# Performance work log

Measured on AMD Instinct MI355X. Metric: run time of the kernel, lower is better.

Reference implementation:

```python
import jax, jax.numpy as jnp
import numpy as np

NUM_BLOCKS = 10  # dilation doubling cycle
NUM_LAYERS = 4   # total blocks = 40


def _dconv(x, w, b, d):
    """Causal dilated conv1d, kernel=2. x:[B,C,T], w:[O,I,2] -> [B,O,T].
    Torch pads (d,d) then slices off the last d frames == left-pad by d."""
    y = jax.lax.conv_general_dilated(
        x, w, window_strides=(1,), padding=[(d, 0)], rhs_dilation=(d,),
        dimension_numbers=("NCH", "OIH", "NCH"))
    return y + b[:, None]


def _pw(x, w, b):
    """1x1 conv. x:[B,I,T], w:[O,I,1] -> [B,O,T]."""
    return jnp.einsum("oi,bit->bot", w[:, :, 0], x) + b[:, None]


def setup_inputs() -> dict:
    key = jax.random.key(0)
    ks = jax.random.split(key, 16)
    s = 0.05
    return {
        "x": jax.random.normal(ks[0], (8, 256, 16384), jnp.float32),
        "in_w": jax.random.normal(ks[1], (32, 256, 1), jnp.float32) * s,
        "in_b": jax.random.normal(ks[2], (32,), jnp.float32) * s,
        "conv_w": jax.random.normal(ks[3], (40, 32, 32, 2), jnp.float32) * s,
        "conv_b": jax.random.normal(ks[4], (40, 32), jnp.float32) * s,
        "gate_w": jax.random.normal(ks[5], (40, 32, 32, 2), jnp.float32) * s,
        "gate_b": jax.random.normal(ks[6], (40, 32), jnp.float32) * s,
        "res_w": jax.random.normal(ks[7], (40, 32, 32, 1), jnp.float32) * s,
        "res_b": jax.random.normal(ks[8], (40, 32), jnp.float32) * s,
        "skip_w": jax.random.normal(ks[9], (40, 32, 32, 1), jnp.float32) * s,
        "skip_b": jax.random.normal(ks[10], (40, 32), jnp.float32) * s,
        "s1_w": jax.random.normal(ks[11], (32, 32, 1), jnp.float32) * s,
        "s1_b": jax.random.normal(ks[12], (32,), jnp.float32) * s,
        "s2_w": jax.random.normal(ks[13], (256, 32, 1), jnp.float32) * s,
        "s2_b": jax.random.normal(ks[14], (256,), jnp.float32) * s,
    }


def reference(x, in_w, in_b, conv_w, conv_b, gate_w, gate_b,
              res_w, res_b, skip_w, skip_b, s1_w, s1_b, s2_w, s2_b):
    h = _pw(x, in_w, in_b)  # [B,32,T]
    skip_sum = jnp.zeros_like(h)
    for i in range(NUM_LAYERS * NUM_BLOCKS):
        d = 2 ** (i % NUM_BLOCKS)
        a = jnp.tanh(_dconv(h, conv_w[i], conv_b[i], d)) * \
            jax.nn.sigmoid(_dconv(h, gate_w[i], gate_b[i], d))
        h = h + _pw(a, res_w[i], res_b[i])
        skip_sum = skip_sum + _pw(a, skip_w[i], skip_b[i])
    out = jax.nn.relu(_pw(skip_sum, s1_w, s1_b))
    out = _pw(out, s2_w, s2_b)  # [B,256,T]
    return out
```

## Files before the change

### kernel.cpp

```cpp
#include <hip/hip_runtime.h>

#define T_LEN 16384

typedef _Float16 f16;
typedef f16 f16x8 __attribute__((ext_vector_type(8)));
typedef float f32x4 __attribute__((ext_vector_type(4)));

__device__ __forceinline__ float fast_exp2(float x) { return __builtin_amdgcn_exp2f(x); }
__device__ __forceinline__ float fast_rcp(float x)  { return __builtin_amdgcn_rcpf(x); }
__device__ __forceinline__ float fast_tanh(float x) {
  return 1.f - 2.f * fast_rcp(1.f + fast_exp2(x * 2.885390081777927f));
}
__device__ __forceinline__ float fast_sig(float x) {
  return fast_rcp(1.f + fast_exp2(-x * 1.4426950408889634f));
}

__device__ __forceinline__ f32x4 mfma16(f16x8 a, f16x8 b, f32x4 c) {
  return __builtin_amdgcn_mfma_f32_16x16x32_f16(a, b, c, 0, 0, 0);
}

struct h2s { f16 hi, lo; };
__device__ __forceinline__ h2s split(float v) {
  h2s r; r.hi = (f16)v; r.lo = (f16)(v - (float)r.hi); return r;
}


__global__ __launch_bounds__(256, 2) void in_k(
    const float* __restrict__ x, const float* __restrict__ w,
    const float* __restrict__ bias, float4* __restrict__ h, float4* __restrict__ skip)
{
  __shared__ float4 W[256][8];
  __shared__ float B[32];
  const int tid = threadIdx.x;
  for (int i = tid; i < 2048; i += 256) {
    int c = i >> 3, o4 = i & 7;
    W[c][o4] = make_float4(w[(o4*4+0)*256 + c], w[(o4*4+1)*256 + c],
                           w[(o4*4+2)*256 + c], w[(o4*4+3)*256 + c]);
  }
  if (tid < 32) B[tid] = bias[tid];
  __syncthreads();

  const int idx = blockIdx.x * 256 + tid;
  const int b = idx >> 14;
  const int t = idx & (T_LEN - 1);
  const float* xb = x + (size_t)b * 256 * T_LEN + t;

  float acc[32];
  #pragma unroll
  for (int o = 0; o < 32; o++) acc[o] = B[o];
  #pragma unroll 4
  for (int c = 0; c < 256; c++) {
    float v = xb[(size_t)c * T_LEN];
    #pragma unroll
    for (int o4 = 0; o4 < 8; o4++) {
      float4 ww = W[c][o4];
      acc[o4*4+0] += ww.x * v; acc[o4*4+1] += ww.y * v;
      acc[o4*4+2] += ww.z * v; acc[o4*4+3] += ww.w * v;
    }
  }
  #pragma unroll
  for (int j = 0; j < 8; j++) {
    size_t p = ((size_t)(b * 8 + j) << 14) + t;
    h[p]    = make_float4(acc[j*4+0], acc[j*4+1], acc[j*4+2], acc[j*4+3]);
    skip[p] = make_float4(0.f, 0.f, 0.f, 0.f);
  }
}

__global__ __launch_bounds__(256, 1) void layer_k(
    const float4* __restrict__ hin, float4* __restrict__ hout, float4* __restrict__ skip,
    const float* __restrict__ cw, const float* __restrict__ cb,
    const float* __restrict__ gw, const float* __restrict__ gb,
    const float* __restrict__ rw, const float* __restrict__ rb,
    const float* __restrict__ sw, const float* __restrict__ sb, int d)
{
  const int tid  = threadIdx.x;
  const int lane = tid & 63;
  const int g    = lane >> 4;
  const int m16  = lane & 15;

  f16x8 wch[2][2], wcl[2][2], wgh[2][2], wgl[2][2];
  f16x8 wrh[2], wrl[2], wsh[2], wsl[2];
  f32x4 cbv[2], gbv[2], rbv[2], sbv[2];
  #pragma unroll
  for (int mt = 0; mt < 2; mt++) {
    const int o = mt*16 + m16;
    const float4* cp = (const float4*)&cw[(o*32 + 8*g)*2];
    const float4* gp = (const float4*)&gw[(o*32 + 8*g)*2];
    float4 c0=cp[0], c1=cp[1], c2=cp[2], c3=cp[3];
    float4 g0=gp[0], g1=gp[1], g2=gp[2], g3=gp[3];
    float4 r0 = *(const float4*)&rw[o*32 + 8*g];
    float4 r1 = *(const float4*)&rw[o*32 + 8*g + 4];
    float4 s0 = *(const float4*)&sw[o*32 + 8*g];
    float4 s1 = *(const float4*)&sw[o*32 + 8*g + 4];
    float cc[16] = {c0.x,c0.y,c0.z,c0.w, c1.x,c1.y,c1.z,c1.w,
                    c2.x,c2.y,c2.z,c2.w, c3.x,c3.y,c3.z,c3.w};
    float gg[16] = {g0.x,g0.y,g0.z,g0.w, g1.x,g1.y,g1.z,g1.w,
                    g2.x,g2.y,g2.z,g2.w, g3.x,g3.y,g3.z,g3.w};
    float rr[8] = {r0.x,r0.y,r0.z,r0.w, r1.x,r1.y,r1.z,r1.w};
    float ss[8] = {s0.x,s0.y,s0.z,s0.w, s1.x,s1.y,s1.z,s1.w};
    #pragma unroll
    for (int i = 0; i < 8; i++) {
      h2s t0 = split(cc[2*i+0]); wch[mt][0][i]=t0.hi; wcl[mt][0][i]=t0.lo;
      h2s t1 = split(cc[2*i+1]); wch[mt][1][i]=t1.hi; wcl[mt][1][i]=t1.lo;
      h2s u0 = split(gg[2*i+0]); wgh[mt][0][i]=u0.hi; wgl[mt][0][i]=u0.lo;
      h2s u1 = split(gg[2*i+1]); wgh[mt][1][i]=u1.hi; wgl[mt][1][i]=u1.lo;
      h2s vr = split(rr[i]);     wrh[mt][i]=vr.hi;    wrl[mt][i]=vr.lo;
      h2s vs = split(ss[i]);     wsh[mt][i]=vs.hi;    wsl[mt][i]=vs.lo;
    }
    cbv[mt] = *(const f32x4*)&cb[mt*16 + 4*g];
    gbv[mt] = *(const f32x4*)&gb[mt*16 + 4*g];
    rbv[mt] = *(const f32x4*)&rb[mt*16 + 4*g];
    sbv[mt] = *(const f32x4*)&sb[mt*16 + 4*g];
  }

  const int wid   = (blockIdx.x << 2) | (tid >> 6);
  const int tile0 = wid << 2;

  float4 Bst[2][4];
  {
    const int b = tile0 >> 10;
    const int tcol = ((tile0 << 4) & (T_LEN-1)) + m16;
    const size_t cbase = ((size_t)b << 17) + (size_t)tcol;
    Bst[0][0] = hin[cbase + ((size_t)(2*g)   << 14)];
    Bst[0][1] = hin[cbase + ((size_t)(2*g+1) << 14)];
    float4 z = make_float4(0.f,0.f,0.f,0.f);
    Bst[0][2] = z; Bst[0][3] = z;
    if (tcol >= d) {
      Bst[0][2] = hin[cbase - (size_t)d + ((size_t)(2*g)   << 14)];
      Bst[0][3] = hin[cbase - (size_t)d + ((size_t)(2*g+1) << 14)];
    }
  }

  #pragma unroll
  for (int k = 0; k < 4; k++) {
    const int tile = tile0 + k;
    const int b = tile >> 10;
    const int tcol = ((tile << 4) & (T_LEN-1)) + m16;
    const size_t cbase = ((size_t)b << 17) + (size_t)tcol;
    const int cur = k & 1, nxt = cur ^ 1;

    float4 hr0 = hin[cbase  + ((size_t)g     << 14)];
    float4 hr1 = hin[cbase  + ((size_t)(4+g) << 14)];
    float4 sv0 = skip[cbase + ((size_t)g     << 14)];
    float4 sv1 = skip[cbase + ((size_t)(4+g) << 14)];

    f16x8 bth, btl, bdh, bdl;
    {
      float tv[8] = {Bst[cur][0].x,Bst[cur][0].y,Bst[cur][0].z,Bst[cur][0].w,
                     Bst[cur][1].x,Bst[cur][1].y,Bst[cur][1].z,Bst[cur][1].w};
      float dv[8] = {Bst[cur][2].x,Bst[cur][2].y,Bst[cur][2].z,Bst[cur][2].w,
                     Bst[cur][3].x,Bst[cur][3].y,Bst[cur][3].z,Bst[cur][3].w};
      #pragma unroll
      for (int i = 0; i < 8; i++) {
        h2s a = split(tv[i]); bth[i]=a.hi; btl[i]=a.lo;
        h2s c = split(dv[i]); bdh[i]=c.hi; bdl[i]=c.lo;
      }
    }

    if (k < 3) {
      const int tn = tile + 1;
      const int bn = tn >> 10;
      const int tcn = ((tn << 4) & (T_LEN-1)) + m16;
      const size_t cbn = ((size_t)bn << 17) + (size_t)tcn;
      Bst[nxt][0] = hin[cbn + ((size_t)(2*g)   << 14)];
      Bst[nxt][1] = hin[cbn + ((size_t)(2*g+1) << 14)];
      float4 z = make_float4(0.f,0.f,0.f,0.f);
      Bst[nxt][2] = z; Bst[nxt][3] = z;
      if (tcn >= d) {
        Bst[nxt][2] = hin[cbn - (size_t)d + ((size_t)(2*g)   << 14)];
        Bst[nxt][3] = hin[cbn - (size_t)d + ((size_t)(2*g+1) << 14)];
      }
    }

    f32x4 pa[2], ga[2];
    #pragma unroll
    for (int mt = 0; mt < 2; mt++) {
      f32x4 p = {0.f,0.f,0.f,0.f};
      p = mfma16(wch[mt][0], bdh, p);
      p = mfma16(wcl[mt][0], bdh, p);
      p = mfma16(wch[mt][0], bdl, p);
      p = mfma16(wch[mt][1], bth, p);
      p = mfma16(wcl[mt][1], bth, p);
      p = mfma16(wch[mt][1], btl, p);
      pa[mt] = p;
      f32x4 q = {0.f,0.f,0.f,0.f};
      q = mfma16(wgh[mt][0], bdh, q);
      q = mfma16(wgl[mt][0], bdh, q);
      q = mfma16(wgh[mt][0], bdl, q);
      q = mfma16(wgh[mt][1], bth, q);
      q = mfma16(wgl[mt][1], bth, q);
      q = mfma16(wgh[mt][1], btl, q);
      ga[mt] = q;
    }

    float av0[4], av1[4];
    #pragma unroll
    for (int r = 0; r < 4; r++) {
      av0[r] = fast_tanh(pa[0][r] + cbv[0][r]) * fast_sig(ga[0][r] + gbv[0][r]);
      av1[r] = fast_tanh(pa[1][r] + cbv[1][r]) * fast_sig(ga[1][r] + gbv[1][r]);
    }

    f16x8 bah, bal;
    #pragma unroll
    for (int i = 0; i < 8; i++) {
      int srcl = (((2*g + (i>>2)) & 3) << 4) | m16;
      float v0 = __shfl(av0[i&3], srcl, 64);
      float v1 = __shfl(av1[i&3], srcl, 64);
      float v = (g >= 2) ? v1 : v0;
      h2s s = split(v); bah[i]=s.hi; bal[i]=s.lo;
    }

    f32x4 ra[2], sa[2];
    #pragma unroll
    for (int mt = 0; mt < 2; mt++) {
      f32x4 p = {0.f,0.f,0.f,0.f};
      p = mfma16(wrh[mt], bah, p);
      p = mfma16(wrl[mt], bah, p);
      p = mfma16(wrh[mt], bal, p);
      ra[mt] = p;
      f32x4 q = {0.f,0.f,0.f,0.f};
      q = mfma16(wsh[mt], bah, q);
      q = mfma16(wsl[mt], bah, q);
      q = mfma16(wsh[mt], bal, q);
      sa[mt] = q;
    }

    #pragma unroll
    for (int mt = 0; mt < 2; mt++) {
      size_t qidx = cbase + ((size_t)(4*mt + g) << 14);
      float4 hr = (mt == 0) ? hr0 : hr1;
      float4 sv = (mt == 0) ? sv0 : sv1;
      hout[qidx] = make_float4(hr.x + rbv[mt][0] + ra[mt][0],
                               hr.y + rbv[mt][1] + ra[mt][1],
                               hr.z + rbv[mt][2] + ra[mt][2],
                               hr.w + rbv[mt][3] + ra[mt][3]);
      skip[qidx] = make_float4(sv.x + sbv[mt][0] + sa[mt][0],
                               sv.y + sbv[mt][1] + sa[mt][1],
                               sv.z + sbv[mt][2] + sa[mt][2],
                               sv.w + sbv[mt][3] + sa[mt][3]);
    }
  }
}

__global__ __launch_bounds__(256, 2) void out_k(
    const float4* __restrict__ skip,
    const float* __restrict__ w1, const float* __restrict__ b1,
    const float* __restrict__ w2, const float* __restrict__ b2,
    float* __restrict__ out)
{
  __shared__ float4 W1[32][8];
  __shared__ float4 W2[32][64];
  __shared__ float B1[32];
  __shared__ float B2[256];
  const int tid = threadIdx.x;
  {
    int ic = tid >> 3, o4 = tid & 7;
    W1[ic][o4] = make_float4(w1[(o4*4+0)*32+ic], w1[(o4*4+1)*32+ic],
                             w1[(o4*4+2)*32+ic], w1[(o4*4+3)*32+ic]);
  }
  for (int e = tid; e < 2048; e += 256) {
    int ic = e >> 6, o4 = e & 63;
    W2[ic][o4] = make_float4(w2[(o4*4+0)*32+ic], w2[(o4*4+1)*32+ic],
                             w2[(o4*4+2)*32+ic], w2[(o4*4+3)*32+ic]);
  }
  B2[tid & 255] = b2[tid & 255];
  if (tid < 32) B1[tid] = b1[tid];
  __syncthreads();

  const int idx = blockIdx.x * 256 + tid;
  const int b = idx >> 14;
  const int t = idx & (T_LEN - 1);
  const size_t base = ((size_t)b * 8 << 14) + t;

  float sk[32];
  #pragma unroll
  for (int j = 0; j < 8; j++) {
    float4 v = skip[base + ((size_t)j << 14)];
    sk[j*4+0]=v.x; sk[j*4+1]=v.y; sk[j*4+2]=v.z; sk[j*4+3]=v.w;
  }

  float r[32];
  #pragma unroll
  for (int o = 0; o < 32; o++) r[o] = B1[o];
  #pragma unroll
  for (int ic = 0; ic < 32; ic++) {
    float v = sk[ic];
    #pragma unroll
    for (int o4 = 0; o4 < 8; o4++) {
      float4 w = W1[ic][o4];
      r[o4*4+0] += w.x * v; r[o4*4+1] += w.y * v;
      r[o4*4+2] += w.z * v; r[o4*4+3] += w.w * v;
    }
  }
  #pragma unroll
  for (int o = 0; o < 32; o++) r[o] = fmaxf(r[o], 0.f);

  float* ob = out + (size_t)b * 256 * T_LEN + t;
  #pragma unroll 2
  for (int o4 = 0; o4 < 64; o4++) {
    float a0 = B2[o4*4+0], a1 = B2[o4*4+1], a2 = B2[o4*4+2], a3 = B2[o4*4+3];
    #pragma unroll
    for (int ic = 0; ic < 32; ic++) {
      float4 w = W2[ic][o4];
      float v = r[ic];
      a0 += w.x * v; a1 += w.y * v; a2 += w.z * v; a3 += w.w * v;
    }
    ob[(size_t)(o4*4+0)*T_LEN] = a0;
    ob[(size_t)(o4*4+1)*T_LEN] = a1;
    ob[(size_t)(o4*4+2)*T_LEN] = a2;
    ob[(size_t)(o4*4+3)*T_LEN] = a3;
  }
}

extern "C" void kernel_launch(void* const* d_in, const int* in_sizes, int n_in,
                              void* d_out, int out_size, void* d_ws, size_t ws_size,
                              hipStream_t stream)
{
  const float* x    = (const float*)d_in[0];
  const float* in_w = (const float*)d_in[1];
  const float* in_b = (const float*)d_in[2];
  const float* cw   = (const float*)d_in[3];
  const float* cb   = (const float*)d_in[4];
  const float* gw   = (const float*)d_in[5];
  const float* gb   = (const float*)d_in[6];
  const float* rw   = (const float*)d_in[7];
  const float* rb   = (const float*)d_in[8];
  const float* sw   = (const float*)d_in[9];
  const float* sb   = (const float*)d_in[10];
  const float* w1   = (const float*)d_in[11];
  const float* b1   = (const float*)d_in[12];
  const float* w2   = (const float*)d_in[13];
  const float* b2   = (const float*)d_in[14];
  float* out = (float*)d_out;

  float4* h0   = (float4*)out;
  float4* h1   = (float4*)(out + 4194304);
  float4* skip = (float4*)d_ws;

  dim3 blk(256);
  in_k<<<dim3(512), blk, 0, stream>>>(x, in_w, in_b, h0, skip);

  float4* ha = h0;
  float4* hb = h1;
  for (int l = 0; l < 40; l++) {
    int d = 1 << (l % 10);
    layer_k<<<dim3(512), blk, 0, stream>>>(ha, hb, skip,
        cw + (size_t)l * 2048, cb + l * 32,
        gw + (size_t)l * 2048, gb + l * 32,
        rw + (size_t)l * 1024, rb + l * 32,
        sw + (size_t)l * 1024, sb + l * 32, d);
    float4* tmp = ha; ha = hb; hb = tmp;
  }

  out_k<<<dim3(512), blk, 0, stream>>>(skip, w1, b1, w2, b2, out);
}
```

Baseline: 1.213 ms.

## Move input and output pointwise convs to split-fp16 MFMA and swizzle layer blocks

Rewrites the input 1x1 conv (256->32) and the output head (32->32 relu ->256) from scalar FMA loops over LDS-staged weights to 16x16x32 f16 MFMA. Weights and activations are split into hi/lo halves, and three MFMAs per tile approximate fp32 accuracy. Weights now live in registers and the LDS staging is removed. It also swizzles the block index in the layer kernel to change the order in which blocks touch memory. The cost is more register pressure and extra conversion arithmetic, and the output head does strided 4-byte stores.

New measurement: 1.176 ms. 3.1% less time.

```diff
diff --git a/kernel.cpp b/kernel.cpp
--- a/kernel.cpp
+++ b/kernel.cpp
@@ -25,44 +25,72 @@
 }
 
 
-__global__ __launch_bounds__(256, 2) void in_k(
+__global__ __launch_bounds__(256, 1) void in_k(
     const float* __restrict__ x, const float* __restrict__ w,
     const float* __restrict__ bias, float4* __restrict__ h, float4* __restrict__ skip)
 {
-  __shared__ float4 W[256][8];
-  __shared__ float B[32];
-  const int tid = threadIdx.x;
-  for (int i = tid; i < 2048; i += 256) {
-    int c = i >> 3, o4 = i & 7;
-    W[c][o4] = make_float4(w[(o4*4+0)*256 + c], w[(o4*4+1)*256 + c],
-                           w[(o4*4+2)*256 + c], w[(o4*4+3)*256 + c]);
-  }
-  if (tid < 32) B[tid] = bias[tid];
-  __syncthreads();
-
-  const int idx = blockIdx.x * 256 + tid;
-  const int b = idx >> 14;
-  const int t = idx & (T_LEN - 1);
-  const float* xb = x + (size_t)b * 256 * T_LEN + t;
-
-  float acc[32];
-  #pragma unroll
-  for (int o = 0; o < 32; o++) acc[o] = B[o];
-  #pragma unroll 4
-  for (int c = 0; c < 256; c++) {
-    float v = xb[(size_t)c * T_LEN];
-    #pragma unroll
-    for (int o4 = 0; o4 < 8; o4++) {
-      float4 ww = W[c][o4];
-      acc[o4*4+0] += ww.x * v; acc[o4*4+1] += ww.y * v;
-      acc[o4*4+2] += ww.z * v; acc[o4*4+3] += ww.w * v;
-    }
-  }
-  #pragma unroll
-  for (int j = 0; j < 8; j++) {
-    size_t p = ((size_t)(b * 8 + j) << 14) + t;
-    h[p]    = make_float4(acc[j*4+0], acc[j*4+1], acc[j*4+2], acc[j*4+3]);
-    skip[p] = make_float4(0.f, 0.f, 0.f, 0.f);
+  const int tid  = threadIdx.x;
+  const int lane = tid & 63;
+  const int g    = lane >> 4;
+  const int m16  = lane & 15;
+
+  f16x8 wh[2][8], wl[2][8];
+  #pragma unroll
+  for (int mt = 0; mt < 2; mt++) {
+    #pragma unroll
+    for (int kt = 0; kt < 8; kt++) {
+      const float4* wp = (const float4*)&w[(mt*16 + m16)*256 + kt*32 + 8*g];
+      float4 w0 = wp[0], w1 = wp[1];
+      float ww[8] = {w0.x,w0.y,w0.z,w0.w, w1.x,w1.y,w1.z,w1.w};
+      #pragma unroll
+      for (int i = 0; i < 8; i++) {
+        h2s s = split(ww[i]); wh[mt][kt][i] = s.hi; wl[mt][kt][i] = s.lo;
+      }
+    }
+  }
+  f32x4 bv[2];
+  bv[0] = *(const f32x4*)&bias[4*g];
+  bv[1] = *(const f32x4*)&bias[16 + 4*g];
+
+  const int wid   = (blockIdx.x << 2) | (tid >> 6);
+  const int tile0 = wid << 2;
+
+  #pragma unroll
+  for (int k = 0; k < 4; k++) {
+    const int tile = tile0 + k;
+    const int b    = tile >> 10;
+    const int tcol = ((tile << 4) & (T_LEN - 1)) + m16;
+    const float* xb = x + (size_t)b * 256 * T_LEN + tcol;
+
+    float tv[8][8];
+    #pragma unroll
+    for (int kt = 0; kt < 8; kt++)
+      #pragma unroll
+      for (int i = 0; i < 8; i++)
+        tv[kt][i] = xb[(size_t)(kt*32 + 8*g + i) * T_LEN];
+
+    f32x4 acc[2] = {bv[0], bv[1]};
+    #pragma unroll
+    for (int kt = 0; kt < 8; kt++) {
+      f16x8 bh, bl;
+      #pragma unroll
+      for (int i = 0; i < 8; i++) { h2s s = split(tv[kt][i]); bh[i]=s.hi; bl[i]=s.lo; }
+      #pragma unroll
+      for (int mt = 0; mt < 2; mt++) {
+        acc[mt] = mfma16(wh[mt][kt], bh, acc[mt]);
+        acc[mt] = mfma16(wl[mt][kt], bh, acc[mt]);
+        acc[mt] = mfma16(wh[mt][kt], bl, acc[mt]);
+      }
+    }
+
+    const size_t cbase = ((size_t)b << 17) + (size_t)tcol;
+    const float4 z = make_float4(0.f, 0.f, 0.f, 0.f);
+    #pragma unroll
+    for (int mt = 0; mt < 2; mt++) {
+      size_t qidx = cbase + ((size_t)(4*mt + g) << 14);
+      h[qidx]    = make_float4(acc[mt][0], acc[mt][1], acc[mt][2], acc[mt][3]);
+      skip[qidx] = z;
+    }
   }
 }
 
@@ -113,7 +141,9 @@
     sbv[mt] = *(const f32x4*)&sb[mt*16 + 4*g];
   }
 
-  const int wid   = (blockIdx.x << 2) | (tid >> 6);
+  const int bid = blockIdx.x;
+  const int swz = ((bid & 7) << 6) | (bid >> 3);
+  const int wid   = (swz << 2) | (tid >> 6);
   const int tile0 = wid << 2;
 
   float4 Bst[2][4];
@@ -242,73 +272,84 @@
   }
 }
 
-__global__ __launch_bounds__(256, 2) void out_k(
+__global__ __launch_bounds__(256, 1) void out_k(
     const float4* __restrict__ skip,
     const float* __restrict__ w1, const float* __restrict__ b1,
     const float* __restrict__ w2, const float* __restrict__ b2,
     float* __restrict__ out)
 {
-  __shared__ float4 W1[32][8];
-  __shared__ float4 W2[32][64];
-  __shared__ float B1[32];
-  __shared__ float B2[256];
-  const int tid = threadIdx.x;
-  {
-    int ic = tid >> 3, o4 = tid & 7;
-    W1[ic][o4] = make_float4(w1[(o4*4+0)*32+ic], w1[(o4*4+1)*32+ic],
-                             w1[(o4*4+2)*32+ic], w1[(o4*4+3)*32+ic]);
-  }
-  for (int e = tid; e < 2048; e += 256) {
-    int ic = e >> 6, o4 = e & 63;
-    W2[ic][o4] = make_float4(w2[(o4*4+0)*32+ic], w2[(o4*4+1)*32+ic],
-                             w2[(o4*4+2)*32+ic], w2[(o4*4+3)*32+ic]);
-  }
-  B2[tid & 255] = b2[tid & 255];
-  if (tid < 32) B1[tid] = b1[tid];
-  __syncthreads();
-
-  const int idx = blockIdx.x * 256 + tid;
-  const int b = idx >> 14;
-  const int t = idx & (T_LEN - 1);
-  const size_t base = ((size_t)b * 8 << 14) + t;
-
-  float sk[32];
-  #pragma unroll
-  for (int j = 0; j < 8; j++) {
-    float4 v = skip[base + ((size_t)j << 14)];
-    sk[j*4+0]=v.x; sk[j*4+1]=v.y; sk[j*4+2]=v.z; sk[j*4+3]=v.w;
-  }
-
-  float r[32];
-  #pragma unroll
-  for (int o = 0; o < 32; o++) r[o] = B1[o];
-  #pragma unroll
-  for (int ic = 0; ic < 32; ic++) {
-    float v = sk[ic];
-    #pragma unroll
-    for (int o4 = 0; o4 < 8; o4++) {
-      float4 w = W1[ic][o4];
-      r[o4*4+0] += w.x * v; r[o4*4+1] += w.y * v;
-      r[o4*4+2] += w.z * v; r[o4*4+3] += w.w * v;
-    }
-  }
-  #pragma unroll
-  for (int o = 0; o < 32; o++) r[o] = fmaxf(r[o], 0.f);
-
-  float* ob = out + (size_t)b * 256 * T_LEN + t;
-  #pragma unroll 2
-  for (int o4 = 0; o4 < 64; o4++) {
-    float a0 = B2[o4*4+0], a1 = B2[o4*4+1], a2 = B2[o4*4+2], a3 = B2[o4*4+3];
-    #pragma unroll
-    for (int ic = 0; ic < 32; ic++) {
-      float4 w = W2[ic][o4];
-      float v = r[ic];
-      a0 += w.x * v; a1 += w.y * v; a2 += w.z * v; a3 += w.w * v;
-    }
-    ob[(size_t)(o4*4+0)*T_LEN] = a0;
-    ob[(size_t)(o4*4+1)*T_LEN] = a1;
-    ob[(size_t)(o4*4+2)*T_LEN] = a2;
-    ob[(size_t)(o4*4+3)*T_LEN] = a3;
+  const int tid  = threadIdx.x;
+  const int lane = tid & 63;
+  const int g    = lane >> 4;
+  const int m16  = lane & 15;
+
+  f16x8 w1h[2], w1l[2];
+  #pragma unroll
+  for (int mt = 0; mt < 2; mt++) {
+    const float4* wp = (const float4*)&w1[(mt*16 + m16)*32 + 8*g];
+    float4 a0 = wp[0], a1 = wp[1];
+    float ww[8] = {a0.x,a0.y,a0.z,a0.w, a1.x,a1.y,a1.z,a1.w};
+    #pragma unroll
+    for (int i = 0; i < 8; i++) { h2s s = split(ww[i]); w1h[mt][i]=s.hi; w1l[mt][i]=s.lo; }
+  }
+  f16x8 w2h[16], w2l[16];
+  #pragma unroll
+  for (int mt = 0; mt < 16; mt++) {
+    const float4* wp = (const float4*)&w2[(mt*16 + m16)*32 + 8*g];
+    float4 a0 = wp[0], a1 = wp[1];
+    float ww[8] = {a0.x,a0.y,a0.z,a0.w, a1.x,a1.y,a1.z,a1.w};
+    #pragma unroll
+    for (int i = 0; i < 8; i++) { h2s s = split(ww[i]); w2h[mt][i]=s.hi; w2l[mt][i]=s.lo; }
+  }
+  f32x4 b1v[2];
+  b1v[0] = *(const f32x4*)&b1[4*g];
+  b1v[1] = *(const f32x4*)&b1[16 + 4*g];
+
+  const int wid   = (blockIdx.x << 2) | (tid >> 6);
+  const int tile0 = wid << 2;
+
+  #pragma unroll
+  for (int k = 0; k < 4; k++) {
+    const int tile = tile0 + k;
+    const int b    = tile >> 10;
+    const int tcol = ((tile << 4) & (T_LEN - 1)) + m16;
+    const size_t cbase = ((size_t)b << 17) + (size_t)tcol;
+
+    float4 q0 = skip[cbase + ((size_t)(2*g)   << 14)];
+    float4 q1 = skip[cbase + ((size_t)(2*g+1) << 14)];
+    float sv[8] = {q0.x,q0.y,q0.z,q0.w, q1.x,q1.y,q1.z,q1.w};
+    f16x8 bh, bl;
+    #pragma unroll
+    for (int i = 0; i < 8; i++) { h2s s = split(sv[i]); bh[i]=s.hi; bl[i]=s.lo; }
+
+    f32x4 c0 = b1v[0], c1 = b1v[1];
+    c0 = mfma16(w1h[0], bh, c0); c0 = mfma16(w1l[0], bh, c0); c0 = mfma16(w1h[0], bl, c0);
+    c1 = mfma16(w1h[1], bh, c1); c1 = mfma16(w1l[1], bh, c1); c1 = mfma16(w1h[1], bl, c1);
+    float r0[4], r1[4];
+    #pragma unroll
+    for (int r = 0; r < 4; r++) { r0[r] = fmaxf(c0[r], 0.f); r1[r] = fmaxf(c1[r], 0.f); }
+
+    f16x8 rh, rl;
+    #pragma unroll
+    for (int i = 0; i < 8; i++) {
+      int srcl = (((2*g + (i>>2)) & 3) << 4) | m16;
+      float v0 = __shfl(r0[i&3], srcl, 64);
+      float v1 = __shfl(r1[i&3], srcl, 64);
+      float v = (g >= 2) ? v1 : v0;
+      h2s s = split(v); rh[i]=s.hi; rl[i]=s.lo;
+    }
+
+    float* ob = out + (size_t)b * 256 * T_LEN + tcol;
+    #pragma unroll
+    for (int mt = 0; mt < 16; mt++) {
+      f32x4 c = *(const f32x4*)&b2[mt*16 + 4*g];
+      c = mfma16(w2h[mt], rh, c);
+      c = mfma16(w2l[mt], rh, c);
+      c = mfma16(w2h[mt], rl, c);
+      #pragma unroll
+      for (int r = 0; r < 4; r++)
+        ob[(size_t)(mt*16 + 4*g + r) * T_LEN] = c[r];
+    }
   }
 }
 
```
